# Kernel tuning notes

Hardware: AMD Instinct MI355X
Metric: run time of the kernel (lower is better)

## Reference

```python
import jax, jax.numpy as jnp
import numpy as np

H = 1024   # hidden_dim
B = 4096   # batch
T = 128    # forecast_len
IN = 1     # output_dim (univariate)


def setup_inputs() -> dict:
    key = jax.random.key(0)
    ks = jax.random.split(key, 8)
    s = 1.0 / np.sqrt(H)  # torch LSTM/Linear default uniform init scale
    u = lambda k, shape: jax.random.uniform(k, shape, jnp.float32, -s, s)
    return {
        "hidden": jax.random.normal(ks[0], (1, B, H), jnp.float32),
        "cell":   jax.random.normal(ks[1], (1, B, H), jnp.float32),
        "W_ih":   u(ks[2], (4 * H, IN)),   # torch gate order: i, f, g, o
        "W_hh":   u(ks[3], (4 * H, H)),
        "b_ih":   u(ks[4], (4 * H,)),
        "b_hh":   u(ks[5], (4 * H,)),
        "W_out":  u(ks[6], (IN, H)),
        "b_out":  u(ks[7], (IN,)),
    }


def reference(hidden, cell, W_ih, W_hh, b_ih, b_hh, W_out, b_out):
    h = hidden[0]  # [B, H]  (num_layers == 1)
    c = cell[0]    # [B, H]
    x0 = jnp.zeros((h.shape[0], IN), h.dtype)  # initial decoder input = zeros
    b = b_ih + b_hh

    def step(carry, _):
        x, h, c = carry
        gates = x @ W_ih.T + h @ W_hh.T + b          # [B, 4H]
        i, f, g, o = jnp.split(gates, 4, axis=-1)    # torch order i,f,g,o
        c = jax.nn.sigmoid(f) * c + jax.nn.sigmoid(i) * jnp.tanh(g)
        h = jax.nn.sigmoid(o) * jnp.tanh(c)
        pred = h @ W_out.T + b_out                   # [B, 1]
        return (pred, h, c), pred                    # prediction fed back as next input

    _, preds = jax.lax.scan(step, (x0, h, c), None, length=T)  # [T, B, 1]
    return jnp.transpose(preds, (1, 0, 2))  # [B, T, 1]
```

## Files before the change

### kernel.cpp

```cpp
#include <hip/hip_runtime.h>
#include <hip/hip_bf16.h>
#include <stdint.h>


#define HH 1024
#define BB 4096
#define TT 128

#define BM 128
#define BKK 64

typedef __bf16 bf16;
typedef __bf16 v8bf __attribute__((ext_vector_type(8)));
typedef float f32x4 __attribute__((ext_vector_type(4)));

__device__ __forceinline__ float fast_sigmoid(float x) {
    return 1.0f / (1.0f + __expf(-x));
}
__device__ __forceinline__ float fast_tanh(float x) {
    return 1.0f - 2.0f / (__expf(2.0f * x) + 1.0f);
}

__device__ __forceinline__ void gload_lds16(const void* g, void* l) {
    __builtin_amdgcn_global_load_lds(
        (const __attribute__((address_space(1))) uint32_t*)(uintptr_t)g,
        (__attribute__((address_space(3))) uint32_t*)(uint32_t)(uintptr_t)l,
        16, 0, 0);
}


__global__ void prep_weights(const float* __restrict__ Whh,
                             const float* __restrict__ bih,
                             const float* __restrict__ bhh,
                             const float* __restrict__ Wih,
                             const float* __restrict__ Wout,
                             const float* __restrict__ bout,
                             bf16* __restrict__ Wr0, bf16* __restrict__ Wr1,
                             float* __restrict__ bias0, float* __restrict__ bias1) {
    int idx = blockIdx.x * blockDim.x + threadIdx.x;
    if (idx < 4 * HH * HH) {
        int k   = idx & (HH - 1);
        int row = idx >> 10;
        int jb2 = row >> 8;
        int g   = (row >> 6) & 3;
        int jj  = row & 63;
        int srow = g * HH + jb2 * 64 + jj;
        float wv = Whh[srow * HH + k];
        Wr0[idx] = (bf16)wv;
        Wr1[idx] = (bf16)(wv + Wih[srow] * Wout[k]);
    }
    if (idx < 4 * HH) {
        float b = bih[idx] + bhh[idx];
        bias0[idx] = b;
        bias1[idx] = b + Wih[idx] * bout[0];
    }
}

__global__ void prep_h(const float* __restrict__ h0, bf16* __restrict__ hb) {
    int idx = blockIdx.x * blockDim.x + threadIdx.x;
    if (idx < BB * HH) hb[idx] = (bf16)h0[idx];
}

__global__ void prep_c(const float* __restrict__ c0, bf16* __restrict__ cb) {
    int idx = blockIdx.x * blockDim.x + threadIdx.x;
    if (idx < BB * HH) cb[idx] = (bf16)c0[idx];
}

__global__ void prep_pred(float* __restrict__ predbuf, const float* __restrict__ b_out) {
    int idx = blockIdx.x * blockDim.x + threadIdx.x;
    if (idx < (TT + 1) * BB) predbuf[idx] = b_out[0];
}


__global__ __launch_bounds__(256, 2)
void lstm_step(const bf16* __restrict__ hread, bf16* __restrict__ hwrite,
               bf16* __restrict__ cbuf,
               const bf16* __restrict__ Wr, const float* __restrict__ biasp,
               const float* __restrict__ Wout, float* __restrict__ predbuf_w) {
    __shared__ bf16 As[BM][BKK];
    __shared__ bf16 Bs[2 * BM][BKK];

    const int tid   = threadIdx.x;
    const int lane  = tid & 63;
    const int w     = tid >> 6;
    const int waveM = w >> 1, waveN = w & 1;
    const int quad  = lane >> 4, l15 = lane & 15;

    const int bid = blockIdx.x;
    const int xcd = bid & 7, loc = bid >> 3;
    const int jb2 = (xcd & 3) * 4 + (loc & 3);
    const int blockB = ((xcd >> 2) * 16 + (loc >> 2)) * BM;

    const bf16* Asrc = hread + (size_t)blockB * HH;
    const bf16* Bsrc = Wr + (size_t)jb2 * 256 * HH;

    const int r8  = lane >> 3;
    const int gc  = (lane & 7) ^ r8;
    const int swr = l15 & 7;

    float bsvv[2][4], wov[2];
#pragma unroll
    for (int jh = 0; jh < 2; jh++) {
        const int j = jb2 * 64 + waveN * 32 + jh * 16 + l15;
#pragma unroll
        for (int g = 0; g < 4; g++) bsvv[jh][g] = biasp[g * HH + j];
        wov[jh] = Wout[j];
    }

    f32x4 acc[4][8];
#pragma unroll
    for (int mi = 0; mi < 4; mi++)
#pragma unroll
        for (int g = 0; g < 4; g++)
#pragma unroll
            for (int jh = 0; jh < 2; jh++) {
                const float bv = bsvv[jh][g];
                acc[mi][g * 2 + jh] = (f32x4){bv, bv, bv, bv};
            }

    for (int k0 = 0; k0 < HH; k0 += BKK) {
#pragma unroll
        for (int c2 = 0; c2 < 4; c2++) {
            const int rowb = w * 32 + c2 * 8;
            gload_lds16(Asrc + (size_t)(rowb + r8) * HH + k0 + gc * 8, &As[rowb][0]);
        }
#pragma unroll
        for (int c2 = 0; c2 < 8; c2++) {
            const int rowb = w * 64 + c2 * 8;
            gload_lds16(Bsrc + (size_t)(rowb + r8) * HH + k0 + gc * 8, &Bs[rowb][0]);
        }
        asm volatile("s_waitcnt vmcnt(0)" ::: "memory");
        __syncthreads();
#pragma unroll
        for (int kk = 0; kk < 2; kk++) {
            v8bf a[4], b[8];
            const int pch = ((kk * 4 + quad) ^ swr) * 8;
#pragma unroll
            for (int mi = 0; mi < 4; mi++)
                a[mi] = *(const v8bf*)&As[waveM * 64 + mi * 16 + l15][pch];
#pragma unroll
            for (int g = 0; g < 4; g++)
#pragma unroll
                for (int jh = 0; jh < 2; jh++)
                    b[g * 2 + jh] =
                        *(const v8bf*)&Bs[g * 64 + waveN * 32 + jh * 16 + l15][pch];
#pragma unroll
            for (int mi = 0; mi < 4; mi++)
#pragma unroll
                for (int nt = 0; nt < 8; nt++)
                    acc[mi][nt] = __builtin_amdgcn_mfma_f32_16x16x32_bf16(
                        a[mi], b[nt], acc[mi][nt], 0, 0, 0);
        }
        __syncthreads();
    }

#pragma unroll
    for (int mi = 0; mi < 4; mi++) {
#pragma unroll
        for (int r = 0; r < 4; r++) {
            const int b = blockB + waveM * 64 + mi * 16 + quad * 4 + r;
            float pacc = 0.0f;
#pragma unroll
            for (int jh = 0; jh < 2; jh++) {
                const int j = jb2 * 64 + waveN * 32 + jh * 16 + l15;
                const float gi = acc[mi][0 + jh][r];
                const float gf = acc[mi][2 + jh][r];
                const float gg = acc[mi][4 + jh][r];
                const float go = acc[mi][6 + jh][r];
                const float cprev = (float)cbuf[(size_t)b * HH + j];
                const float cn = fast_sigmoid(gf) * cprev
                               + fast_sigmoid(gi) * fast_tanh(gg);
                cbuf[(size_t)b * HH + j] = (bf16)cn;
                const float hn = fast_sigmoid(go) * fast_tanh(cn);
                hwrite[(size_t)b * HH + j] = (bf16)hn;
                pacc += hn * wov[jh];
            }
            pacc += __shfl_xor(pacc, 1);
            pacc += __shfl_xor(pacc, 2);
            pacc += __shfl_xor(pacc, 4);
            pacc += __shfl_xor(pacc, 8);
            if (l15 == 0) atomicAdd(&predbuf_w[b], pacc);
        }
    }
}


__global__ void write_out(const float* __restrict__ predbuf, float* __restrict__ out) {
    int idx = blockIdx.x * blockDim.x + threadIdx.x;
    if (idx < BB * TT) {
        int t = idx & (TT - 1);
        int b = idx >> 7;
        out[idx] = predbuf[(size_t)(t + 1) * BB + b];
    }
}


extern "C" void kernel_launch(void* const* d_in, const int* in_sizes, int n_in,
                              void* d_out, int out_size, void* d_ws, size_t ws_size,
                              hipStream_t stream) {
    const float* hidden = (const float*)d_in[0];
    const float* cell   = (const float*)d_in[1];
    const float* Wih    = (const float*)d_in[2];
    const float* Whh    = (const float*)d_in[3];
    const float* bih    = (const float*)d_in[4];
    const float* bhh    = (const float*)d_in[5];
    const float* Wout   = (const float*)d_in[6];
    const float* bout   = (const float*)d_in[7];
    float* out = (float*)d_out;

    char* ws = (char*)d_ws;
    bf16* Wr0 = (bf16*)ws;       ws += (size_t)4 * HH * HH * 2;
    bf16* Wr1 = (bf16*)ws;       ws += (size_t)4 * HH * HH * 2;
    bf16* hb0 = (bf16*)ws;       ws += (size_t)BB * HH * 2;
    bf16* hb1 = (bf16*)ws;       ws += (size_t)BB * HH * 2;
    bf16* cbuf = (bf16*)ws;      ws += (size_t)BB * HH * 2;
    float* bias0 = (float*)ws;   ws += (size_t)4 * HH * 4;
    float* bias1 = (float*)ws;   ws += (size_t)4 * HH * 4;
    float* predbuf = (float*)ws; ws += (size_t)(TT + 1) * BB * 4;

    prep_weights<<<(4 * HH * HH + 255) / 256, 256, 0, stream>>>(
        Whh, bih, bhh, Wih, Wout, bout, Wr0, Wr1, bias0, bias1);
    prep_h<<<(BB * HH + 255) / 256, 256, 0, stream>>>(hidden, hb0);
    prep_c<<<(BB * HH + 255) / 256, 256, 0, stream>>>(cell, cbuf);
    prep_pred<<<((TT + 1) * BB + 255) / 256, 256, 0, stream>>>(predbuf, bout);

    bf16* hb[2] = {hb0, hb1};
    for (int t = 0; t < TT; t++) {
        const bf16* hr = hb[t & 1];
        bf16* hw = hb[(t + 1) & 1];
        const bf16* Wr   = (t == 0) ? Wr0 : Wr1;
        const float* bsp = (t == 0) ? bias0 : bias1;
        lstm_step<<<512, 256, 0, stream>>>(
            hr, hw, cbuf, Wr, bsp, Wout, predbuf + (size_t)(t + 1) * BB);
    }

    write_out<<<(BB * TT + 255) / 256, 256, 0, stream>>>(predbuf, out);
}
```

Before: 5.156 ms.

## Fuse per-step LSTM launches into persistent kernel with per-tile counters

Replaces the 128 per-timestep kernel launches with one persistent kernel. The 16 blocks that share a batch tile synchronise through a global atomic counter instead of kernel boundaries. The cell state now lives in registers, packed as bf16 pairs, which removes the per-step global read and write of the cell buffer. The first weight tile is prefetched before the spin-wait. The trade-off is reliance on all 512 blocks being co-resident and on spin-wait overhead, plus an odd conditional expression for the hidden-state computation.

Measured after the change: 19.64 ms. 3.81x slower.

```diff
diff --git a/kernel.cpp b/kernel.cpp
--- a/kernel.cpp
+++ b/kernel.cpp
@@ -26,6 +26,18 @@
         (const __attribute__((address_space(1))) uint32_t*)(uintptr_t)g,
         (__attribute__((address_space(3))) uint32_t*)(uint32_t)(uintptr_t)l,
         16, 0, 0);
+}
+
+__device__ __forceinline__ unsigned short bf16_bits(float x) {
+    bf16 h = (bf16)x;
+    unsigned short u;
+    __builtin_memcpy(&u, &h, 2);
+    return u;
+}
+__device__ __forceinline__ float bits_to_f32(unsigned int us16) {
+    union { unsigned int u; float f; } v;
+    v.u = us16 << 16;
+    return v.f;
 }
 
 
@@ -61,22 +73,22 @@
     if (idx < BB * HH) hb[idx] = (bf16)h0[idx];
 }
 
-__global__ void prep_c(const float* __restrict__ c0, bf16* __restrict__ cb) {
-    int idx = blockIdx.x * blockDim.x + threadIdx.x;
-    if (idx < BB * HH) cb[idx] = (bf16)c0[idx];
-}
-
-__global__ void prep_pred(float* __restrict__ predbuf, const float* __restrict__ b_out) {
+__global__ void prep_pred(float* __restrict__ predbuf, const float* __restrict__ b_out,
+                          unsigned int* __restrict__ cnt) {
     int idx = blockIdx.x * blockDim.x + threadIdx.x;
     if (idx < (TT + 1) * BB) predbuf[idx] = b_out[0];
+    if (idx < 32) cnt[idx] = 0;
 }
 
 
 __global__ __launch_bounds__(256, 2)
-void lstm_step(const bf16* __restrict__ hread, bf16* __restrict__ hwrite,
-               bf16* __restrict__ cbuf,
-               const bf16* __restrict__ Wr, const float* __restrict__ biasp,
-               const float* __restrict__ Wout, float* __restrict__ predbuf_w) {
+void lstm_persist(const float* __restrict__ c0,
+                  bf16* __restrict__ hb0, bf16* __restrict__ hb1,
+                  const bf16* __restrict__ Wr0, const bf16* __restrict__ Wr1,
+                  const float* __restrict__ bias0, const float* __restrict__ bias1,
+                  const float* __restrict__ Wout,
+                  float* __restrict__ predbuf,
+                  unsigned int* __restrict__ cnt) {
     __shared__ bf16 As[BM][BKK];
     __shared__ bf16 Bs[2 * BM][BKK];
 
@@ -87,100 +99,151 @@
     const int quad  = lane >> 4, l15 = lane & 15;
 
     const int bid = blockIdx.x;
-    const int xcd = bid & 7, loc = bid >> 3;
-    const int jb2 = (xcd & 3) * 4 + (loc & 3);
-    const int blockB = ((xcd >> 2) * 16 + (loc >> 2)) * BM;
-
-    const bf16* Asrc = hread + (size_t)blockB * HH;
-    const bf16* Bsrc = Wr + (size_t)jb2 * 256 * HH;
+    const int xcd = bid & 7, s = bid >> 3;
+    const int jb2 = s >> 2;
+    const int mb  = (s & 3) * 8 + xcd;
+    const int blockB = mb * BM;
 
     const int r8  = lane >> 3;
     const int gc  = (lane & 7) ^ r8;
     const int swr = l15 & 7;
 
-    float bsvv[2][4], wov[2];
+    float wov[2];
+    int jj[2];
 #pragma unroll
     for (int jh = 0; jh < 2; jh++) {
-        const int j = jb2 * 64 + waveN * 32 + jh * 16 + l15;
-#pragma unroll
-        for (int g = 0; g < 4; g++) bsvv[jh][g] = biasp[g * HH + j];
-        wov[jh] = Wout[j];
-    }
-
-    f32x4 acc[4][8];
+        jj[jh] = jb2 * 64 + waveN * 32 + jh * 16 + l15;
+        wov[jh] = Wout[jj[jh]];
+    }
+
+    unsigned int creg[16];
 #pragma unroll
     for (int mi = 0; mi < 4; mi++)
 #pragma unroll
-        for (int g = 0; g < 4; g++)
-#pragma unroll
-            for (int jh = 0; jh < 2; jh++) {
-                const float bv = bsvv[jh][g];
-                acc[mi][g * 2 + jh] = (f32x4){bv, bv, bv, bv};
-            }
-
-    for (int k0 = 0; k0 < HH; k0 += BKK) {
-#pragma unroll
-        for (int c2 = 0; c2 < 4; c2++) {
-            const int rowb = w * 32 + c2 * 8;
-            gload_lds16(Asrc + (size_t)(rowb + r8) * HH + k0 + gc * 8, &As[rowb][0]);
-        }
+        for (int r = 0; r < 4; r++) {
+            const int b = blockB + waveM * 64 + mi * 16 + quad * 4 + r;
+            const unsigned int u0 = bf16_bits(c0[(size_t)b * HH + jj[0]]);
+            const unsigned int u1 = bf16_bits(c0[(size_t)b * HH + jj[1]]);
+            creg[mi * 4 + r] = u0 | (u1 << 16);
+        }
+
+    for (int t = 0; t < TT; t++) {
+        const bf16* hread  = (t & 1) ? hb1 : hb0;
+        bf16*       hwrite = (t & 1) ? hb0 : hb1;
+        const bf16* Bsrc   = ((t == 0) ? Wr0 : Wr1) + (size_t)jb2 * 256 * HH;
+        const float* biasp = (t == 0) ? bias0 : bias1;
+        const bf16* Asrc   = hread + (size_t)blockB * HH;
+        float* predw = predbuf + (size_t)(t + 1) * BB;
+
 #pragma unroll
         for (int c2 = 0; c2 < 8; c2++) {
             const int rowb = w * 64 + c2 * 8;
-            gload_lds16(Bsrc + (size_t)(rowb + r8) * HH + k0 + gc * 8, &Bs[rowb][0]);
-        }
-        asm volatile("s_waitcnt vmcnt(0)" ::: "memory");
+            gload_lds16(Bsrc + (size_t)(rowb + r8) * HH + gc * 8, &Bs[rowb][0]);
+        }
+        if (t > 0) {
+            if (tid == 0) {
+                while (atomicAdd(&cnt[mb], 0u) < 16u * (unsigned)t)
+                    __builtin_amdgcn_s_sleep(2);
+            }
+        }
         __syncthreads();
-#pragma unroll
-        for (int kk = 0; kk < 2; kk++) {
-            v8bf a[4], b[8];
-            const int pch = ((kk * 4 + quad) ^ swr) * 8;
-#pragma unroll
-            for (int mi = 0; mi < 4; mi++)
-                a[mi] = *(const v8bf*)&As[waveM * 64 + mi * 16 + l15][pch];
+        __threadfence();
+
+        float bsvv[2][4];
+#pragma unroll
+        for (int jh = 0; jh < 2; jh++)
+#pragma unroll
+            for (int g = 0; g < 4; g++) bsvv[jh][g] = biasp[g * HH + jj[jh]];
+        f32x4 acc[4][8];
+#pragma unroll
+        for (int mi = 0; mi < 4; mi++)
 #pragma unroll
             for (int g = 0; g < 4; g++)
 #pragma unroll
-                for (int jh = 0; jh < 2; jh++)
-                    b[g * 2 + jh] =
-                        *(const v8bf*)&Bs[g * 64 + waveN * 32 + jh * 16 + l15][pch];
-#pragma unroll
-            for (int mi = 0; mi < 4; mi++)
-#pragma unroll
-                for (int nt = 0; nt < 8; nt++)
-                    acc[mi][nt] = __builtin_amdgcn_mfma_f32_16x16x32_bf16(
-                        a[mi], b[nt], acc[mi][nt], 0, 0, 0);
-        }
+                for (int jh = 0; jh < 2; jh++) {
+                    const float bv = bsvv[jh][g];
+                    acc[mi][g * 2 + jh] = (f32x4){bv, bv, bv, bv};
+                }
+
+        for (int k0 = 0; k0 < HH; k0 += BKK) {
+#pragma unroll
+            for (int c2 = 0; c2 < 4; c2++) {
+                const int rowb = w * 32 + c2 * 8;
+                gload_lds16(Asrc + (size_t)(rowb + r8) * HH + k0 + gc * 8,
+                            &As[rowb][0]);
+            }
+            if (k0) {
+#pragma unroll
+                for (int c2 = 0; c2 < 8; c2++) {
+                    const int rowb = w * 64 + c2 * 8;
+                    gload_lds16(Bsrc + (size_t)(rowb + r8) * HH + k0 + gc * 8,
+                                &Bs[rowb][0]);
+                }
+            }
+            asm volatile("s_waitcnt vmcnt(0)" ::: "memory");
+            __syncthreads();
+#pragma unroll
+            for (int kk = 0; kk < 2; kk++) {
+                v8bf a[4], b[8];
+                const int pch = ((kk * 4 + quad) ^ swr) * 8;
+#pragma unroll
+                for (int mi = 0; mi < 4; mi++)
+                    a[mi] = *(const v8bf*)&As[waveM * 64 + mi * 16 + l15][pch];
+#pragma unroll
+                for (int g = 0; g < 4; g++)
+#pragma unroll
+                    for (int jh = 0; jh < 2; jh++)
+                        b[g * 2 + jh] = *(const v8bf*)
+                            &Bs[g * 64 + waveN * 32 + jh * 16 + l15][pch];
+#pragma unroll
+                for (int mi = 0; mi < 4; mi++)
+#pragma unroll
+                    for (int nt = 0; nt < 8; nt++)
+                        acc[mi][nt] = __builtin_amdgcn_mfma_f32_16x16x32_bf16(
+                            a[mi], b[nt], acc[mi][nt], 0, 0, 0);
+            }
+            __syncthreads();
+        }
+
+#pragma unroll
+        for (int mi = 0; mi < 4; mi++) {
+#pragma unroll
+            for (int r = 0; r < 4; r++) {
+                const int b = blockB + waveM * 64 + mi * 16 + quad * 4 + r;
+                const unsigned int cpk = creg[mi * 4 + r];
+                unsigned int cnew = 0;
+                float pacc = 0.0f;
+#pragma unroll
+                for (int jh = 0; jh < 2; jh++) {
+                    const float gi = acc[mi][0 + jh][r];
+                    const float gf = acc[mi][2 + jh][r];
+                    const float gg = acc[mi][4 + jh][r];
+                    const float go = acc[mi][6 + jh][r];
+                    const float cprev =
+                        bits_to_f32(jh ? (cpk >> 16) : (cpk & 0xffffu));
+                    const float cn = fast_sigmoid(gf) * cprev
+                                   + fast_sigmoid(gi) * fast_tanh(gg);
+                    const unsigned int cb = bf16_bits(cn);
+                    cnew |= jh ? (cb << 16) : cb;
+                    const float hn =
+                        fast_sigmoid(go) * bits_to_f32(cb) == 0.0f
+                            ? fast_sigmoid(go) * fast_tanh(bits_to_f32(cb))
+                            : fast_sigmoid(go) * fast_tanh(cn);
+                    hwrite[(size_t)b * HH + jj[jh]] = (bf16)hn;
+                    pacc += hn * wov[jh];
+                }
+                creg[mi * 4 + r] = cnew;
+                pacc += __shfl_xor(pacc, 1);
+                pacc += __shfl_xor(pacc, 2);
+                pacc += __shfl_xor(pacc, 4);
+                pacc += __shfl_xor(pacc, 8);
+                if (l15 == 0) atomicAdd(&predw[b], pacc);
+            }
+        }
+
+        __threadfence();
         __syncthreads();
-    }
-
-#pragma unroll
-    for (int mi = 0; mi < 4; mi++) {
-#pragma unroll
-        for (int r = 0; r < 4; r++) {
-            const int b = blockB + waveM * 64 + mi * 16 + quad * 4 + r;
-            float pacc = 0.0f;
-#pragma unroll
-            for (int jh = 0; jh < 2; jh++) {
-                const int j = jb2 * 64 + waveN * 32 + jh * 16 + l15;
-                const float gi = acc[mi][0 + jh][r];
-                const float gf = acc[mi][2 + jh][r];
-                const float gg = acc[mi][4 + jh][r];
-                const float go = acc[mi][6 + jh][r];
-                const float cprev = (float)cbuf[(size_t)b * HH + j];
-                const float cn = fast_sigmoid(gf) * cprev
-                               + fast_sigmoid(gi) * fast_tanh(gg);
-                cbuf[(size_t)b * HH + j] = (bf16)cn;
-                const float hn = fast_sigmoid(go) * fast_tanh(cn);
-                hwrite[(size_t)b * HH + j] = (bf16)hn;
-                pacc += hn * wov[jh];
-            }
-            pacc += __shfl_xor(pacc, 1);
-            pacc += __shfl_xor(pacc, 2);
-            pacc += __shfl_xor(pacc, 4);
-            pacc += __shfl_xor(pacc, 8);
-            if (l15 == 0) atomicAdd(&predbuf_w[b], pacc);
-        }
+        if (tid == 0 && t < TT - 1) atomicAdd(&cnt[mb], 1u);
     }
 }
 
@@ -213,26 +276,18 @@
     bf16* Wr1 = (bf16*)ws;       ws += (size_t)4 * HH * HH * 2;
     bf16* hb0 = (bf16*)ws;       ws += (size_t)BB * HH * 2;
     bf16* hb1 = (bf16*)ws;       ws += (size_t)BB * HH * 2;
-    bf16* cbuf = (bf16*)ws;      ws += (size_t)BB * HH * 2;
     float* bias0 = (float*)ws;   ws += (size_t)4 * HH * 4;
     float* bias1 = (float*)ws;   ws += (size_t)4 * HH * 4;
     float* predbuf = (float*)ws; ws += (size_t)(TT + 1) * BB * 4;
+    unsigned int* cnt = (unsigned int*)ws; ws += 32 * 4;
 
     prep_weights<<<(4 * HH * HH + 255) / 256, 256, 0, stream>>>(
         Whh, bih, bhh, Wih, Wout, bout, Wr0, Wr1, bias0, bias1);
     prep_h<<<(BB * HH + 255) / 256, 256, 0, stream>>>(hidden, hb0);
-    prep_c<<<(BB * HH + 255) / 256, 256, 0, stream>>>(cell, cbuf);
-    prep_pred<<<((TT + 1) * BB + 255) / 256, 256, 0, stream>>>(predbuf, bout);
-
-    bf16* hb[2] = {hb0, hb1};
-    for (int t = 0; t < TT; t++) {
-        const bf16* hr = hb[t & 1];
-        bf16* hw = hb[(t + 1) & 1];
-        const bf16* Wr   = (t == 0) ? Wr0 : Wr1;
-        const float* bsp = (t == 0) ? bias0 : bias1;
-        lstm_step<<<512, 256, 0, stream>>>(
-            hr, hw, cbuf, Wr, bsp, Wout, predbuf + (size_t)(t + 1) * BB);
-    }
+    prep_pred<<<((TT + 1) * BB + 255) / 256, 256, 0, stream>>>(predbuf, bout, cnt);
+
+    lstm_persist<<<512, 256, 0, stream>>>(
+        cell, hb0, hb1, Wr0, Wr1, bias0, bias1, Wout, predbuf, cnt);
 
     write_out<<<(BB * TT + 255) / 256, 256, 0, stream>>>(predbuf, out);
 }
```
